# Performance work log

Measured on AMD Instinct MI355X. Metric: run time of the kernel, lower is better.

## Reference

```python
import math
import jax, jax.numpy as jnp
import numpy as np

D_MODEL = 2048
NUM_HEADS = 16
D_HEAD = D_MODEL // NUM_HEADS
THETA = 10000.0


def _rope_tables(seq_len, d_head):
    # interleaved-pair RoPE tables, shape (seq, d_head//2)
    idx = jnp.arange(0, d_head, 2, dtype=jnp.float32)
    inv_freq = THETA ** (-idx / d_head)
    angles = jnp.arange(seq_len, dtype=jnp.float32)[:, None] * inv_freq[None, :]
    return jnp.cos(angles), jnp.sin(angles)


def _apply_rope(x, cos, sin):
    # x: (B, H, S, d_head); cos/sin: (S, d_head//2)
    B, H, S, d = x.shape
    xp = x.reshape(B, H, S, d // 2, 2)
    xe, xo = xp[..., 0], xp[..., 1]
    rot = jnp.stack([xe * cos - xo * sin, xe * sin + xo * cos], axis=-1)
    return rot.reshape(B, H, S, d)


def setup_inputs() -> dict:
    key = jax.random.key(0)
    k_x, k_q, k_k, k_v, k_o = jax.random.split(key, 5)
    std = math.sqrt(2.0 / (D_MODEL + D_MODEL))
    x = jax.random.normal(k_x, (4, 2048, D_MODEL), dtype=jnp.float32)
    Wq = jax.random.normal(k_q, (D_MODEL, D_MODEL), dtype=jnp.float32) * std
    Wk = jax.random.normal(k_k, (D_MODEL, D_MODEL), dtype=jnp.float32) * std
    Wv = jax.random.normal(k_v, (D_MODEL, D_MODEL), dtype=jnp.float32) * std
    Wo = jax.random.normal(k_o, (D_MODEL, D_MODEL), dtype=jnp.float32) * std
    return {"x": x, "Wq": Wq, "Wk": Wk, "Wv": Wv, "Wo": Wo}


def reference(x, Wq, Wk, Wv, Wo):
    B, S, D = x.shape
    H, dh = NUM_HEADS, D_HEAD
    # projections: weight stored (out, in), y = x @ W^T
    def proj(W):
        y = jnp.einsum('bsi,oi->bso', x, W)
        return y.reshape(B, S, H, dh).transpose(0, 2, 1, 3)  # (B,H,S,dh)
    q, k, v = proj(Wq), proj(Wk), proj(Wv)

    cos, sin = _rope_tables(S, dh)
    q = _apply_rope(q, cos, sin)
    k = _apply_rope(k, cos, sin)

    # naive fp32 attention with causal mask
    scores = jnp.einsum('bhqd,bhkd->bhqk', q.astype(jnp.float32), k.astype(jnp.float32)) / math.sqrt(dh)
    causal = jnp.tril(jnp.ones((S, S), dtype=bool))
    scores = jnp.where(causal, scores, jnp.finfo(jnp.float32).min)
    probs = jax.nn.softmax(scores, axis=-1).astype(v.dtype)
    attn = jnp.einsum('bhqk,bhkd->bhqd', probs, v)

    attn = attn.transpose(0, 2, 1, 3).reshape(B, S, D)
    return jnp.einsum('bsi,oi->bso', attn, Wo)
```

## Files before the change

kernel.cpp:

```cpp
#include <hip/hip_runtime.h>

typedef float f32x4 __attribute__((ext_vector_type(4)));
typedef _Float16 f16x8 __attribute__((ext_vector_type(8)));
typedef unsigned short u16x8 __attribute__((ext_vector_type(8)));
typedef unsigned short u16x4 __attribute__((ext_vector_type(4)));

#define KD 2048

static __device__ __forceinline__ unsigned short f2h(float f) {
    _Float16 h = (_Float16)f;
    return __builtin_bit_cast(unsigned short, h);
}
static __device__ __forceinline__ void gl16(const unsigned short* g, unsigned short* l) {
    __builtin_amdgcn_global_load_lds(
        (const __attribute__((address_space(1))) unsigned int*)g,
        (__attribute__((address_space(3))) unsigned int*)l, 16, 0, 0);
}

__global__ void rope_tables(float* __restrict__ cosT, float* __restrict__ sinT) {
    int i = blockIdx.x * 256 + threadIdx.x;
    if (i >= 2048 * 64) return;
    int s = i >> 6, j = i & 63;
    float freq = exp2f(-(2.0f * (float)j / 128.0f) * 13.287712379549449f);
    float a = (float)s * freq;
    cosT[i] = cosf(a);
    sinT[i] = sinf(a);
}

__global__ void precvt_all(const float* __restrict__ x,
                           const float* __restrict__ Wq, const float* __restrict__ Wk,
                           const float* __restrict__ Wv, const float* __restrict__ Wo,
                           unsigned short* __restrict__ xh,
                           unsigned short* __restrict__ Wqh, unsigned short* __restrict__ Wkh,
                           unsigned short* __restrict__ Wvh, unsigned short* __restrict__ Woh) {
    int i = blockIdx.x * 256 + threadIdx.x;
    const float* s; unsigned short* d; int off;
    if (i < 4194304) { s = x; d = xh; off = i; }
    else {
        int j = i - 4194304; int m = j >> 20; off = j & 1048575;
        s = m == 0 ? Wq : m == 1 ? Wk : m == 2 ? Wv : Wo;
        d = m == 0 ? Wqh : m == 1 ? Wkh : m == 2 ? Wvh : Woh;
    }
    f32x4 v = ((const f32x4*)s)[off];
    u16x4 h = { f2h(v[0]), f2h(v[1]), f2h(v[2]), f2h(v[3]) };
    ((u16x4*)d)[off] = h;
}

__global__ __launch_bounds__(256)
void gemm_qkv(const unsigned short* __restrict__ xh,
              const unsigned short* __restrict__ Wqh, const unsigned short* __restrict__ Wkh,
              const unsigned short* __restrict__ Wvh,
              unsigned short* __restrict__ Qh, unsigned short* __restrict__ Kh,
              unsigned short* __restrict__ Vt,
              const float* __restrict__ cosT, const float* __restrict__ sinT)
{
    const int bid = blockIdx.x;
    const int mode = bid >> 10;
    const int r = bid & 1023;
    int bi, bj;
    const unsigned short *Ah, *Bh;
    if (mode <= 1) { bi = r >> 6; bj = r & 63; Ah = mode ? Wkh : Wqh; Bh = xh; }
    else           { bi = r >> 4; bj = r & 15; Ah = xh;              Bh = Wvh; }

    const int tid = threadIdx.x;
    const int lane = tid & 63;
    const int w = tid >> 6;
    const int wm = w >> 1, wn = w & 1;
    const int lg = lane >> 4, lr = lane & 15;

    __shared__ unsigned short As[2][128 * 32];
    __shared__ unsigned short Bs[2][128 * 32];

    f32x4 acc[4][4];
#pragma unroll
    for (int i = 0; i < 4; ++i)
#pragma unroll
        for (int j = 0; j < 4; ++j) acc[i][j] = f32x4{0.f, 0.f, 0.f, 0.f};

    const int srow = lane >> 2;
    const int schk = (lane & 3) ^ ((lane >> 4) & 3);

    auto stage = [&](int k0, int buf) {
#pragma unroll
        for (int q2 = 0; q2 < 2; ++q2) {
            const int seg = w * 2 + q2;
            const int row = seg * 16 + srow;
            const int loff = seg * 512 + lane * 8;
            const size_t ga = (size_t)(bi * 128 + row) * KD + k0 + schk * 8;
            const size_t gb = (size_t)(bj * 128 + row) * KD + k0 + schk * 8;
            gl16(Ah + ga, &As[buf][loff]);
            gl16(Bh + gb, &Bs[buf][loff]);
        }
    };
    const int roff = 8 * (lg ^ ((lr >> 2) & 3));
    auto term = [&](const unsigned short* A_, const unsigned short* B_) {
        const unsigned short* Ap = A_ + (wm * 64 + lr) * 32;
        const unsigned short* Bp = B_ + (wn * 64 + lr) * 32;
        f16x8 af[4], bf[4];
#pragma unroll
        for (int i = 0; i < 4; ++i) {
            af[i] = *(const f16x8*)(Ap + i * 512 + roff);
            bf[i] = *(const f16x8*)(Bp + i * 512 + roff);
        }
#pragma unroll
        for (int mi = 0; mi < 4; ++mi)
#pragma unroll
            for (int ni = 0; ni < 4; ++ni)
                acc[mi][ni] = __builtin_amdgcn_mfma_f32_16x16x32_f16(af[mi], bf[ni], acc[mi][ni], 0, 0, 0);
    };

    stage(0, 0);
#pragma unroll 1
    for (int kt = 0; kt < 64; ++kt) {
        const int cur = kt & 1;
        __syncthreads();
        if (kt < 63) stage((kt + 1) * 32, cur ^ 1);
        term(As[cur], Bs[cur]);
    }

    if (mode <= 1) {
        unsigned short* OH = mode ? Kh : Qh;
        const float scale = mode ? 1.0f : 0.12751743343f;
#pragma unroll
        for (int mi = 0; mi < 4; ++mi) {
            int i0 = bi * 128 + wm * 64 + mi * 16 + lg * 4;
            int h = i0 >> 7, dd = i0 & 127;
            int jp = dd >> 1;
#pragma unroll
            for (int ni = 0; ni < 4; ++ni) {
                int jj = bj * 128 + wn * 64 + ni * 16 + lr;
                int b = jj >> 11, s = jj & 2047;
                float c0 = cosT[s * 64 + jp],     s0 = sinT[s * 64 + jp];
                float c1 = cosT[s * 64 + jp + 1], s1 = sinT[s * 64 + jp + 1];
                f32x4 v = acc[mi][ni];
                float r0 = (v[0] * c0 - v[1] * s0) * scale;
                float r1 = (v[0] * s0 + v[1] * c0) * scale;
                float r2 = (v[2] * c1 - v[3] * s1) * scale;
                float r3 = (v[2] * s1 + v[3] * c1) * scale;
                u16x4 ph = { f2h(r0), f2h(r1), f2h(r2), f2h(r3) };
                *(u16x4*)&OH[((size_t)(b * 16 + h) * 2048 + s) * 128 + dd] = ph;
            }
        }
    } else {
#pragma unroll
        for (int mi = 0; mi < 4; ++mi) {
            int i0 = bi * 128 + wm * 64 + mi * 16 + lg * 4;
            int b = i0 >> 11, s = i0 & 2047;
#pragma unroll
            for (int ni = 0; ni < 4; ++ni) {
                int jj = bj * 128 + wn * 64 + ni * 16 + lr;
                int h = jj >> 7, dd = jj & 127;
                f32x4 v = acc[mi][ni];
                u16x4 pk = { f2h(v[0]), f2h(v[1]), f2h(v[2]), f2h(v[3]) };
                *(u16x4*)&Vt[((size_t)(b * 16 + h) * 128 + dd) * 2048 + s] = pk;
            }
        }
    }
}

__global__ __launch_bounds__(256)
void gemm_o(const unsigned short* __restrict__ Ah, const unsigned short* __restrict__ Bh,
            float* __restrict__ O)
{
    const int bi = blockIdx.x, bj = blockIdx.y;
    const int tid = threadIdx.x;
    const int lane = tid & 63;
    const int w = tid >> 6;
    const int wm = w >> 1, wn = w & 1;
    const int lg = lane >> 4, lr = lane & 15;

    __shared__ unsigned short As[2][128 * 32];
    __shared__ unsigned short Bs[2][128 * 32];

    f32x4 acc[4][4];
#pragma unroll
    for (int i = 0; i < 4; ++i)
#pragma unroll
        for (int j = 0; j < 4; ++j) acc[i][j] = f32x4{0.f, 0.f, 0.f, 0.f};

    const int srow = lane >> 2;
    const int schk = (lane & 3) ^ ((lane >> 4) & 3);

    auto stage = [&](int k0, int buf) {
#pragma unroll
        for (int q2 = 0; q2 < 2; ++q2) {
            const int seg = w * 2 + q2;
            const int row = seg * 16 + srow;
            const int loff = seg * 512 + lane * 8;
            const size_t ga = (size_t)(bi * 128 + row) * KD + k0 + schk * 8;
            const size_t gb = (size_t)(bj * 128 + row) * KD + k0 + schk * 8;
            gl16(Ah + ga, &As[buf][loff]);
            gl16(Bh + gb, &Bs[buf][loff]);
        }
    };
    const int roff = 8 * (lg ^ ((lr >> 2) & 3));
    auto term = [&](const unsigned short* A_, const unsigned short* B_) {
        const unsigned short* Ap = A_ + (wm * 64 + lr) * 32;
        const unsigned short* Bp = B_ + (wn * 64 + lr) * 32;
        f16x8 af[4], bf[4];
#pragma unroll
        for (int i = 0; i < 4; ++i) {
            af[i] = *(const f16x8*)(Ap + i * 512 + roff);
            bf[i] = *(const f16x8*)(Bp + i * 512 + roff);
        }
#pragma unroll
        for (int mi = 0; mi < 4; ++mi)
#pragma unroll
            for (int ni = 0; ni < 4; ++ni)
                acc[mi][ni] = __builtin_amdgcn_mfma_f32_16x16x32_f16(af[mi], bf[ni], acc[mi][ni], 0, 0, 0);
    };

    stage(0, 0);
#pragma unroll 1
    for (int kt = 0; kt < 64; ++kt) {
        const int cur = kt & 1;
        __syncthreads();
        if (kt < 63) stage((kt + 1) * 32, cur ^ 1);
        term(As[cur], Bs[cur]);
    }

#pragma unroll
    for (int mi = 0; mi < 4; ++mi) {
        int i0 = bi * 128 + wm * 64 + mi * 16 + lg * 4;
#pragma unroll
        for (int ni = 0; ni < 4; ++ni) {
            int jj = bj * 128 + wn * 64 + ni * 16 + lr;
            *(f32x4*)&O[(size_t)jj * 2048 + i0] = acc[mi][ni];
        }
    }
}

__global__ __launch_bounds__(256)
void attn7(const unsigned short* __restrict__ Qh, const unsigned short* __restrict__ Kh,
           const unsigned short* __restrict__ Vt, unsigned short* __restrict__ Ob)
{
    const int bid = blockIdx.x;
    const int bh = bid & 63;
    const int p  = bid >> 6;
    const int tid = threadIdx.x;
    const int lane = tid & 63, w = tid >> 6;
    const int lg = lane >> 4, lr = lane & 15;
    const int b = bh >> 4, h = bh & 15;

    __shared__ unsigned short Ks[2][32 * 128];
    __shared__ unsigned short Vs[2][128 * 32];
    __shared__ unsigned short Ps[4][16 * 40];

    auto stage = [&](int t) {
        const int buf = t & 1;
        const int kv0 = t * 32;
#pragma unroll
        for (int q2 = 0; q2 < 2; ++q2) {
            const int seg = w * 2 + q2;
            {
                const int row = seg * 4 + (lane >> 4);
                const int gcol = 8 * ((lane & 15) ^ (row & 7));
                gl16(Kh + ((size_t)bh * 2048 + kv0 + row) * 128 + gcol,
                     &Ks[buf][seg * 512 + lane * 8]);
            }
            {
                const int row = seg * 16 + (lane >> 2);
                const int gcol = 8 * ((lane & 3) ^ ((row >> 1) & 3));
                gl16(Vt + ((size_t)bh * 128 + row) * 2048 + kv0 + gcol,
                     &Vs[buf][seg * 512 + lane * 8]);
            }
        }
    };

#pragma unroll 1
    for (int half = 0; half < 2; ++half) {
        const int qt = half ? p : (31 - p);
        const int qbase = qt * 64 + w * 16;
        const int q = qbase + lr;
        const int t_last = (qbase + 15) >> 5;
        const int nkv = 2 * (qt + 1);

        f16x8 qf[4];
        {
            const size_t qoff = ((size_t)bh * 2048 + q) * 128;
#pragma unroll
            for (int kk = 0; kk < 4; ++kk)
                qf[kk] = *(const f16x8*)(Qh + qoff + kk * 32 + lg * 8);
        }

        f32x4 o[8];
#pragma unroll
        for (int i = 0; i < 8; ++i) o[i] = f32x4{0.f, 0.f, 0.f, 0.f};
        float m_run = -1e30f, l_run = 0.f;

        stage(0);
        __syncthreads();

#pragma unroll 1
        for (int t = 0; t < nkv; ++t) {
            if (t + 1 < nkv) stage(t + 1);
            const int buf = t & 1;
            if (t <= t_last) {
                f32x4 sc[2] = { f32x4{0.f,0.f,0.f,0.f}, f32x4{0.f,0.f,0.f,0.f} };
#pragma unroll
                for (int m2 = 0; m2 < 2; ++m2)
#pragma unroll
                    for (int kk = 0; kk < 4; ++kk) {
                        const int go = 8 * ((4 * kk + lg) ^ (lr & 7));
                        f16x8 kf = *(const f16x8*)&Ks[buf][(m2 * 16 + lr) * 128 + go];
                        sc[m2] = __builtin_amdgcn_mfma_f32_16x16x32_f16(kf, qf[kk], sc[m2], 0, 0, 0);
                    }
                if (t == t_last) {
                    const int kv0 = t * 32;
#pragma unroll
                    for (int m2 = 0; m2 < 2; ++m2)
#pragma unroll
                        for (int rr = 0; rr < 4; ++rr) {
                            int kvg = kv0 + m2 * 16 + lg * 4 + rr;
                            if (kvg > q) sc[m2][rr] = -1e30f;
                        }
                }
                float pmax = fmaxf(fmaxf(fmaxf(sc[0][0], sc[0][1]), fmaxf(sc[0][2], sc[0][3])),
                                   fmaxf(fmaxf(sc[1][0], sc[1][1]), fmaxf(sc[1][2], sc[1][3])));
                pmax = fmaxf(pmax, __shfl_xor(pmax, 16));
                pmax = fmaxf(pmax, __shfl_xor(pmax, 32));
                if (!__all(pmax <= m_run + 11.54f)) {
                    float mnew = fmaxf(m_run, pmax);
                    float alpha = exp2f(m_run - mnew);
                    m_run = mnew;
                    l_run *= alpha;
#pragma unroll
                    for (int ni = 0; ni < 8; ++ni) {
                        o[ni][0] *= alpha; o[ni][1] *= alpha;
                        o[ni][2] *= alpha; o[ni][3] *= alpha;
                    }
                }
                float psum = 0.f;
                u16x4 pq[2];
#pragma unroll
                for (int m2 = 0; m2 < 2; ++m2)
#pragma unroll
                    for (int rr = 0; rr < 4; ++rr) {
                        float pv = exp2f(sc[m2][rr] - m_run);
                        psum += pv;
                        pq[m2][rr] = f2h(pv);
                    }
                l_run += psum;
                *(u16x4*)&Ps[w][lr * 40 + lg * 4]      = pq[0];
                *(u16x4*)&Ps[w][lr * 40 + 16 + lg * 4] = pq[1];
                f16x8 pf = *(const f16x8*)&Ps[w][lr * 40 + lg * 8];
#pragma unroll
                for (int ni = 0; ni < 8; ++ni) {
                    f16x8 vf = *(const f16x8*)&Vs[buf][(ni * 16 + lr) * 32 + 8 * (lg ^ ((lr >> 1) & 3))];
                    o[ni] = __builtin_amdgcn_mfma_f32_16x16x32_f16(vf, pf, o[ni], 0, 0, 0);
                }
            }
            __syncthreads();
        }

        float l = l_run;
        l += __shfl_xor(l, 16);
        l += __shfl_xor(l, 32);
        float inv = 1.f / l;
        unsigned short* Op = Ob + (((size_t)(b * 2048 + q) * 16 + h) * 128);
#pragma unroll
        for (int ni = 0; ni < 8; ++ni) {
            u16x4 pk = { f2h(o[ni][0] * inv), f2h(o[ni][1] * inv),
                         f2h(o[ni][2] * inv), f2h(o[ni][3] * inv) };
            *(u16x4*)&Op[ni * 16 + lg * 4] = pk;
        }
    }
}

extern "C" void kernel_launch(void* const* d_in, const int* in_sizes, int n_in,
                              void* d_out, int out_size, void* d_ws, size_t ws_size,
                              hipStream_t stream) {
    const float* x  = (const float*)d_in[0];
    const float* Wq = (const float*)d_in[1];
    const float* Wk = (const float*)d_in[2];
    const float* Wv = (const float*)d_in[3];
    const float* Wo = (const float*)d_in[4];

    char* ws = (char*)d_ws;
    float* cosT = (float*)ws;
    float* sinT = cosT + 2048 * 64;
    unsigned short* xh  = (unsigned short*)(ws + (1 << 20));
    unsigned short* Vt  = xh  + (size_t)16777216;
    unsigned short* Wqh = Vt  + (size_t)16777216;
    unsigned short* Wkh = Wqh + (size_t)4194304;
    unsigned short* Wvh = Wkh + (size_t)4194304;
    unsigned short* Woh = Wvh + (size_t)4194304;

    unsigned short* attn_b = xh;

    unsigned short* Qh = (unsigned short*)d_out;
    unsigned short* Kh = Qh + (size_t)16777216;

    rope_tables<<<dim3(512), 256, 0, stream>>>(cosT, sinT);
    precvt_all<<<dim3(32768), 256, 0, stream>>>(x, Wq, Wk, Wv, Wo,
                                                xh, Wqh, Wkh, Wvh, Woh);
    gemm_qkv<<<dim3(3072), 256, 0, stream>>>(xh, Wqh, Wkh, Wvh, Qh, Kh, Vt, cosT, sinT);
    attn7<<<dim3(1024), 256, 0, stream>>>(Qh, Kh, Vt, attn_b);
    gemm_o<<<dim3(16, 64), 256, 0, stream>>>(Woh, attn_b, (float*)d_out);
}
```

Before: 588.2 us.

## Triple-buffer LDS staging in projection GEMMs with partial vmcnt waits

Both the QKV projection and the output projection GEMMs move from double to triple buffering in LDS. Loads are issued two tiles ahead, and each iteration waits only for the older tile's loads (vmcnt(4)) rather than doing a full __syncthreads drain. The goal is to hide global-load latency behind MFMA work. In exchange, LDS use per block grows by half, which can lower occupancy, and correctness depends on the hand-written vmcnt count matching the number of loads each stage issues.

```diff
diff --git a/kernel.cpp b/kernel.cpp
--- a/kernel.cpp
+++ b/kernel.cpp
@@ -68,8 +68,8 @@
     const int wm = w >> 1, wn = w & 1;
     const int lg = lane >> 4, lr = lane & 15;
 
-    __shared__ unsigned short As[2][128 * 32];
-    __shared__ unsigned short Bs[2][128 * 32];
+    __shared__ unsigned short As[3][128 * 32];
+    __shared__ unsigned short Bs[3][128 * 32];
 
     f32x4 acc[4][4];
 #pragma unroll
@@ -110,13 +110,24 @@
     };
 
     stage(0, 0);
+    stage(32, 1);
+    int cur = 0;
 #pragma unroll 1
-    for (int kt = 0; kt < 64; ++kt) {
-        const int cur = kt & 1;
-        __syncthreads();
-        if (kt < 63) stage((kt + 1) * 32, cur ^ 1);
+    for (int kt = 0; kt < 63; ++kt) {
+        asm volatile("s_waitcnt vmcnt(4)" ::: "memory");
+        __builtin_amdgcn_s_barrier();
+        __builtin_amdgcn_sched_barrier(0);
+        if (kt < 62) {
+            int nb = cur + 2; if (nb >= 3) nb -= 3;
+            stage((kt + 2) * 32, nb);
+        }
         term(As[cur], Bs[cur]);
-    }
+        if (++cur == 3) cur = 0;
+    }
+    asm volatile("s_waitcnt vmcnt(0)" ::: "memory");
+    __builtin_amdgcn_s_barrier();
+    __builtin_amdgcn_sched_barrier(0);
+    term(As[cur], Bs[cur]);
 
     if (mode <= 1) {
         unsigned short* OH = mode ? Kh : Qh;
@@ -169,8 +180,8 @@
     const int wm = w >> 1, wn = w & 1;
     const int lg = lane >> 4, lr = lane & 15;
 
-    __shared__ unsigned short As[2][128 * 32];
-    __shared__ unsigned short Bs[2][128 * 32];
+    __shared__ unsigned short As[3][128 * 32];
+    __shared__ unsigned short Bs[3][128 * 32];
 
     f32x4 acc[4][4];
 #pragma unroll
@@ -211,13 +222,24 @@
     };
 
     stage(0, 0);
+    stage(32, 1);
+    int cur = 0;
 #pragma unroll 1
-    for (int kt = 0; kt < 64; ++kt) {
-        const int cur = kt & 1;
-        __syncthreads();
-        if (kt < 63) stage((kt + 1) * 32, cur ^ 1);
+    for (int kt = 0; kt < 63; ++kt) {
+        asm volatile("s_waitcnt vmcnt(4)" ::: "memory");
+        __builtin_amdgcn_s_barrier();
+        __builtin_amdgcn_sched_barrier(0);
+        if (kt < 62) {
+            int nb = cur + 2; if (nb >= 3) nb -= 3;
+            stage((kt + 2) * 32, nb);
+        }
         term(As[cur], Bs[cur]);
-    }
+        if (++cur == 3) cur = 0;
+    }
+    asm volatile("s_waitcnt vmcnt(0)" ::: "memory");
+    __builtin_amdgcn_s_barrier();
+    __builtin_amdgcn_sched_barrier(0);
+    term(As[cur], Bs[cur]);
 
 #pragma unroll
     for (int mi = 0; mi < 4; ++mi) {
```

Measured after the change: 608.1 us. 3.4% more time.
